# Performance work log

Hardware: AMD Instinct MI355X
Metric: run time of the kernel (lower is better)

The kernel has to match this reference:

```python
import jax, jax.numpy as jnp
import numpy as np

B = 1024          # graphs
NPG = 258         # nodes per graph (hard-coded in the model's reshape)
N = B * NPG
F_IN = 64
DEG = 8
E = B * NPG * DEG
CH = 32
HID = 128


def setup_inputs() -> dict:
    key = jax.random.key(0)
    ks = jax.random.split(key, 16)
    x = jax.random.normal(ks[0], (N, F_IN), dtype=jnp.float32)
    # within-graph random edges (disjoint batch): local idx in [0,258) + graph offset
    src_l = jax.random.randint(ks[1], (E,), 0, NPG, dtype=jnp.int32)
    dst_l = jax.random.randint(ks[2], (E,), 0, NPG, dtype=jnp.int32)
    offs = jnp.repeat(jnp.arange(B, dtype=jnp.int32) * NPG, NPG * DEG)
    edge_src = src_l + offs
    edge_dst = dst_l + offs
    edge_w = jax.random.uniform(ks[3], (E,), dtype=jnp.float32)
    s = lambda f: 1.0 / np.sqrt(f)
    W0 = jax.random.normal(ks[4], (F_IN, CH), dtype=jnp.float32) * s(F_IN)
    W1 = jax.random.normal(ks[5], (F_IN, CH), dtype=jnp.float32) * s(F_IN)
    b_conv = jnp.zeros((CH,), dtype=jnp.float32)
    Wd1 = jax.random.normal(ks[6], (NPG * CH, HID), dtype=jnp.float32) * s(NPG * CH)
    bd1 = jnp.zeros((HID,), dtype=jnp.float32)
    Wd2 = jax.random.normal(ks[7], (HID, HID // 2), dtype=jnp.float32) * s(HID)
    bd2 = jnp.zeros((HID // 2,), dtype=jnp.float32)
    Wd3 = jax.random.normal(ks[8], (HID // 2, HID // 4), dtype=jnp.float32) * s(HID // 2)
    bd3 = jnp.zeros((HID // 4,), dtype=jnp.float32)
    Wd4 = jax.random.normal(ks[9], (HID // 4, 1), dtype=jnp.float32) * s(HID // 4)
    bd4 = jnp.zeros((1,), dtype=jnp.float32)
    return dict(x=x, edge_src=edge_src, edge_dst=edge_dst, edge_w=edge_w,
                W0=W0, W1=W1, b_conv=b_conv, Wd1=Wd1, bd1=bd1, Wd2=Wd2, bd2=bd2,
                Wd3=Wd3, bd3=bd3, Wd4=Wd4, bd4=bd4)


def reference(x, edge_src, edge_dst, edge_w, W0, W1, b_conv,
              Wd1, bd1, Wd2, bd2, Wd3, bd3, Wd4, bd4):
    n = x.shape[0]
    # ChebConv K=2: T0 = X, T1 = A_hat X ; out = T0 W0 + T1 W1 + b, elu
    ax = jax.ops.segment_sum(edge_w[:, None] * x[edge_src], edge_dst, num_segments=n)
    h = jax.nn.elu(x @ W0 + ax @ W1 + b_conv)          # [N, 32]
    h = h.reshape(n // NPG, NPG * CH)                   # [B, 258*32] (reshape+flatten)
    h = jax.nn.relu(h @ Wd1 + bd1)
    h = jax.nn.relu(h @ Wd2 + bd2)
    # dropout is inactive at inference
    h = jax.nn.relu(h @ Wd3 + bd3)
    out = jax.nn.sigmoid(h @ Wd4 + bd4)                 # [B, 1]
    return out
```

## Files before the change

kernel.cpp:

```cpp
#include <hip/hip_runtime.h>
#include <hip/hip_bf16.h>

#define NPG 258
#define DEG 8
#define EPG 2064
#define CH 32
#define FIN 64
#define NB 1024
#define NTOT (NB * NPG)
#define HID 128
#define KTOT 8256
#define KSPL 32

typedef __attribute__((ext_vector_type(8))) short bf16x8;
typedef __attribute__((ext_vector_type(4))) float f32x4;

__device__ inline unsigned short f2bf(float f) {
    __hip_bfloat16 b = __float2bfloat16(f);
    return __builtin_bit_cast(unsigned short, b);
}
__device__ inline float bf2f(unsigned short u) {
    return __builtin_bit_cast(float, (unsigned)u << 16);
}
__device__ inline void cvt_split(const float4 a, const float4 b, bf16x8& hi, bf16x8& lo) {
    float f[8] = {a.x, a.y, a.z, a.w, b.x, b.y, b.z, b.w};
#pragma unroll
    for (int j = 0; j < 8; ++j) {
        unsigned short h = f2bf(f[j]);
        hi[j] = (short)h;
        lo[j] = (short)f2bf(f[j] - bf2f(h));
    }
}

__global__ __launch_bounds__(256) void prep_wcat(
    const float* __restrict__ W0, const float* __restrict__ W1,
    unsigned short* __restrict__ Wh, unsigned short* __restrict__ Wl)
{
#pragma unroll
    for (int i = 0; i < 16; ++i) {
        const int idx = threadIdx.x + i * 256;
        const int c = idx >> 6, k = idx & 63;
        const float v = (c < 32) ? W0[k * CH + c] : W1[k * CH + (c - 32)];
        const unsigned short h = f2bf(v);
        Wh[c * 64 + k] = h;
        Wl[c * 64 + k] = f2bf(v - bf2f(h));
    }
}

__global__ __launch_bounds__(256) void wd1_transpose(
    const float* __restrict__ Wd1, unsigned short* __restrict__ Wd1T)
{
    __shared__ float st[128][65];
    const int tid = threadIdx.x;
    const int k0 = blockIdx.x * 64;
#pragma unroll
    for (int i = 0; i < 32; ++i) {
        const int idx = tid + i * 256;
        const int kl = idx >> 7, cc = idx & 127;
        st[cc][kl] = Wd1[(size_t)(k0 + kl) * HID + cc];
    }
    __syncthreads();
    const int cc = tid >> 1, gq = tid & 1;
#pragma unroll
    for (int i = 0; i < 8; ++i) {
        const int ko = (gq + i * 2) * 4;
        ushort4 o;
        o.x = f2bf(st[cc][ko + 0]);
        o.y = f2bf(st[cc][ko + 1]);
        o.z = f2bf(st[cc][ko + 2]);
        o.w = f2bf(st[cc][ko + 3]);
        *reinterpret_cast<ushort4*>(Wd1T + (size_t)cc * KTOT + k0 + ko) = o;
    }
}

__global__ __launch_bounds__(256) void conv_gemm(
    const float* __restrict__ x, const unsigned short* __restrict__ Wh,
    const unsigned short* __restrict__ Wl,
    float* __restrict__ y0, unsigned short* __restrict__ y1)
{
    __shared__ unsigned short bsh[64 * 64];
    __shared__ unsigned short bsl[64 * 64];
    const int tid = threadIdx.x;
#pragma unroll
    for (int i = 0; i < 2; ++i) {
        const int s = tid + i * 256;
        const int col = s >> 3, o = s & 7;
        const int so = o ^ (col & 7);
        *reinterpret_cast<uint4*>(&bsh[col * 64 + so * 8]) =
            *reinterpret_cast<const uint4*>(&Wh[col * 64 + o * 8]);
        *reinterpret_cast<uint4*>(&bsl[col * 64 + so * 8]) =
            *reinterpret_cast<const uint4*>(&Wl[col * 64 + o * 8]);
    }
    __syncthreads();

    const int w = tid >> 6, lane = tid & 63;
    const int r = lane & 15, kq = lane >> 4;
    const long rowbase = (long)blockIdx.x * 128 + w * 32;

    bf16x8 ah[2][2], al[2][2];
#pragma unroll
    for (int mt = 0; mt < 2; ++mt)
#pragma unroll
        for (int ks = 0; ks < 2; ++ks) {
            const float* xp = x + (rowbase + mt * 16 + r) * FIN + ks * 32 + kq * 8;
            const float4 p0 = *reinterpret_cast<const float4*>(xp);
            const float4 p1 = *reinterpret_cast<const float4*>(xp + 4);
            cvt_split(p0, p1, ah[mt][ks], al[mt][ks]);
        }

    f32x4 acc[2][4];
#pragma unroll
    for (int mt = 0; mt < 2; ++mt)
#pragma unroll
        for (int nt = 0; nt < 4; ++nt) acc[mt][nt] = f32x4{0.f, 0.f, 0.f, 0.f};

#pragma unroll
    for (int nt = 0; nt < 4; ++nt) {
        const int col = nt * 16 + r;
        const int cs = col & 7;
#pragma unroll
        for (int ks = 0; ks < 2; ++ks) {
            const int g = (ks * 4 + kq) ^ cs;
            const bf16x8 bh = *reinterpret_cast<const bf16x8*>(&bsh[col * 64 + g * 8]);
            const bf16x8 bl = *reinterpret_cast<const bf16x8*>(&bsl[col * 64 + g * 8]);
#pragma unroll
            for (int mt = 0; mt < 2; ++mt) {
                acc[mt][nt] = __builtin_amdgcn_mfma_f32_16x16x32_bf16(ah[mt][ks], bh, acc[mt][nt], 0, 0, 0);
                acc[mt][nt] = __builtin_amdgcn_mfma_f32_16x16x32_bf16(ah[mt][ks], bl, acc[mt][nt], 0, 0, 0);
                acc[mt][nt] = __builtin_amdgcn_mfma_f32_16x16x32_bf16(al[mt][ks], bh, acc[mt][nt], 0, 0, 0);
            }
        }
    }

#pragma unroll
    for (int mt = 0; mt < 2; ++mt)
#pragma unroll
        for (int rr = 0; rr < 4; ++rr) {
            const long rg = rowbase + mt * 16 + kq * 4 + rr;
            y0[rg * CH + r]      = acc[mt][0][rr];
            y0[rg * CH + 16 + r] = acc[mt][1][rr];
            y1[rg * CH + r]      = f2bf(acc[mt][2][rr]);
            y1[rg * CH + 16 + r] = f2bf(acc[mt][3][rr]);
        }
}

__global__ __launch_bounds__(256) void conv_gather(
    const int* __restrict__ esrc, const int* __restrict__ edst,
    const float* __restrict__ ew, const float* __restrict__ y0,
    const unsigned short* __restrict__ y1, const float* __restrict__ bc,
    unsigned short* __restrict__ h)
{
    __shared__ unsigned short y1s[NPG * CH];
    __shared__ unsigned short slot_src[EPG];
    __shared__ float          slot_w[EPG];
    __shared__ int            row_start[NPG + 2];
    __shared__ int            cursor[NPG];

    const int g   = blockIdx.x;
    const int tid = threadIdx.x;
    const int n0  = g * NPG;
    const long eb = (long)g * EPG;
    const long qb = (long)g * (NPG * CH);

    if (tid < NPG) cursor[tid] = 0;
    if (tid + 256 < NPG) cursor[tid + 256] = 0;
    __syncthreads();

    for (int e = tid; e < EPG; e += 256)
        atomicAdd(&cursor[edst[eb + e] - n0], 1);
#pragma unroll
    for (int i = 0; i < 5; ++i) {
        const int q = tid + i * 256;
        if (q < 1032)
            *reinterpret_cast<uint4*>(&y1s[q * 8]) =
                *reinterpret_cast<const uint4*>(&y1[qb + (long)q * 8]);
    }
    __syncthreads();

    if (tid < 64) {
        const int b0 = tid * 5;
        int loc[5], s = 0;
#pragma unroll
        for (int j = 0; j < 5; ++j) {
            const int idx = b0 + j;
            loc[j] = (idx < NPG) ? cursor[idx] : 0;
            s += loc[j];
        }
        int inc = s;
#pragma unroll
        for (int off = 1; off < 64; off <<= 1) {
            const int t = __shfl_up(inc, off, 64);
            if (tid >= off) inc += t;
        }
        int run = inc - s;
#pragma unroll
        for (int j = 0; j < 5; ++j) {
            const int idx = b0 + j;
            if (idx < NPG) { row_start[idx] = run; cursor[idx] = run; }
            run += loc[j];
        }
        if (tid == 63) row_start[NPG] = inc;
    }
    __syncthreads();

    for (int e = tid; e < EPG; e += 256) {
        const int dl = edst[eb + e] - n0;
        const int sl = esrc[eb + e] - n0;
        const float w = ew[eb + e];
        const int pos = atomicAdd(&cursor[dl], 1);
        slot_src[pos] = (unsigned short)sl;
        slot_w[pos] = w;
    }
    __syncthreads();

    const int c = tid & 31;
    const int rgrp = tid >> 5;
#pragma unroll 1
    for (int p = 0; p < 33; ++p) {
        const int n = p * 8 + rgrp;
        if (n >= NPG) break;
        const int pb = row_start[n], pe = row_start[n + 1];
        float acc = 0.f;
        for (int pos = pb; pos < pe; ++pos)
            acc += slot_w[pos] * bf2f(y1s[slot_src[pos] * CH + c]);
        float v = y0[qb + (long)n * CH + c] + bc[c] + acc;
        v = (v > 0.f) ? v : expm1f(v);
        h[qb + (long)n * CH + c] = f2bf(v);
    }
}

__global__ __launch_bounds__(256) void gemm1(
    const unsigned short* __restrict__ h, const unsigned short* __restrict__ Wd1T,
    float* __restrict__ part)
{
    const int tid = threadIdx.x, w = tid >> 6, lane = tid & 63;
    const int r = lane & 15, kq = lane >> 4;
    const long m0 = (long)blockIdx.x * 64;
    const int ks = blockIdx.y;
    const int kb0 = ks * 258 / KSPL, kb1 = (ks + 1) * 258 / KSPL;
    const int c0 = w * 32;

    f32x4 acc[4][2];
#pragma unroll
    for (int a = 0; a < 4; ++a)
#pragma unroll
        for (int b = 0; b < 2; ++b) acc[a][b] = f32x4{0.f, 0.f, 0.f, 0.f};

    const unsigned short* ap = h    + (m0 + r) * KTOT + kq * 8;
    const unsigned short* bp = Wd1T + (long)(c0 + r) * KTOT + kq * 8;

    for (int kb = kb0; kb < kb1; ++kb) {
        const int k = kb * 32;
        const bf16x8 b0 = *reinterpret_cast<const bf16x8*>(bp + k);
        const bf16x8 b1 = *reinterpret_cast<const bf16x8*>(bp + 16 * KTOT + k);
#pragma unroll
        for (int mt = 0; mt < 4; ++mt) {
            const bf16x8 a = *reinterpret_cast<const bf16x8*>(ap + mt * 16 * KTOT + k);
            acc[mt][0] = __builtin_amdgcn_mfma_f32_16x16x32_bf16(a, b0, acc[mt][0], 0, 0, 0);
            acc[mt][1] = __builtin_amdgcn_mfma_f32_16x16x32_bf16(a, b1, acc[mt][1], 0, 0, 0);
        }
    }

    float* p = part + ((long)ks * NB + m0) * HID + c0;
#pragma unroll
    for (int mt = 0; mt < 4; ++mt)
#pragma unroll
        for (int rr = 0; rr < 4; ++rr) {
            const int row = mt * 16 + kq * 4 + rr;
            p[(long)row * HID + r]      = acc[mt][0][rr];
            p[(long)row * HID + 16 + r] = acc[mt][1][rr];
        }
}

__global__ __launch_bounds__(256) void mlp_tail(
    const float* __restrict__ part, const float* __restrict__ bd1,
    const float* __restrict__ Wd2, const float* __restrict__ bd2,
    const float* __restrict__ Wd3, const float* __restrict__ bd3,
    const float* __restrict__ Wd4, const float* __restrict__ bd4,
    float* __restrict__ out)
{
    __shared__ float w2[128 * 64];
    __shared__ float w3[64 * 32];
    __shared__ float w4[32];
    __shared__ float h1s[4][128];
    __shared__ float h2s[4][64];
    __shared__ float h3s[4][32];

    const int tid = threadIdx.x;
    for (int i = tid; i < 128 * 64; i += 256) w2[i] = Wd2[i];
    for (int i = tid; i < 64 * 32; i += 256)  w3[i] = Wd3[i];
    if (tid < 32) w4[tid] = Wd4[tid];

    const int r = tid >> 6;
    const int lane = tid & 63;
    const int row = blockIdx.x * 4 + r;

    float s0 = bd1[lane], s1 = bd1[lane + 64];
#pragma unroll 8
    for (int s = 0; s < KSPL; ++s) {
        const float* p = part + ((long)s * NB + row) * HID;
        s0 += p[lane];
        s1 += p[lane + 64];
    }
    h1s[r][lane]      = fmaxf(s0, 0.f);
    h1s[r][lane + 64] = fmaxf(s1, 0.f);
    __syncthreads();

    float s2 = bd2[lane];
#pragma unroll 8
    for (int k = 0; k < 128; ++k) s2 += h1s[r][k] * w2[k * 64 + lane];
    h2s[r][lane] = fmaxf(s2, 0.f);
    __syncthreads();

    if (lane < 32) {
        float s3 = bd3[lane];
#pragma unroll 8
        for (int k = 0; k < 64; ++k) s3 += h2s[r][k] * w3[k * 32 + lane];
        h3s[r][lane] = fmaxf(s3, 0.f);
    }
    __syncthreads();

    float p4 = (lane < 32) ? h3s[r][lane] * w4[lane] : 0.f;
#pragma unroll
    for (int off = 32; off > 0; off >>= 1) p4 += __shfl_down(p4, off, 64);
    if (lane == 0) out[row] = 1.f / (1.f + expf(-(p4 + bd4[0])));
}

extern "C" void kernel_launch(void* const* d_in, const int* in_sizes, int n_in,
                              void* d_out, int out_size, void* d_ws, size_t ws_size,
                              hipStream_t stream)
{
    const float* x    = (const float*)d_in[0];
    const int*   esrc = (const int*)d_in[1];
    const int*   edst = (const int*)d_in[2];
    const float* ew   = (const float*)d_in[3];
    const float* W0   = (const float*)d_in[4];
    const float* W1   = (const float*)d_in[5];
    const float* bc   = (const float*)d_in[6];
    const float* Wd1  = (const float*)d_in[7];
    const float* bd1  = (const float*)d_in[8];
    const float* Wd2  = (const float*)d_in[9];
    const float* bd2  = (const float*)d_in[10];
    const float* Wd3  = (const float*)d_in[11];
    const float* bd3  = (const float*)d_in[12];
    const float* Wd4  = (const float*)d_in[13];
    const float* bd4  = (const float*)d_in[14];
    float* out = (float*)d_out;

    char* wsb = (char*)d_ws;
    unsigned short* h    = (unsigned short*)wsb;
    unsigned short* wd1t = (unsigned short*)(wsb + 16908288);
    unsigned short* wch  = (unsigned short*)(wsb + 19021824);
    unsigned short* wcl  = (unsigned short*)(wsb + 19030016);
    float*          y0   = (float*)(wsb + 19038208);
    unsigned short* y1   = (unsigned short*)(wsb + 52854784);
    float*          part = (float*)(wsb + 19038208);

    prep_wcat<<<1, 256, 0, stream>>>(W0, W1, wch, wcl);
    wd1_transpose<<<KTOT / 64, 256, 0, stream>>>(Wd1, wd1t);
    conv_gemm<<<NTOT / 128, 256, 0, stream>>>(x, wch, wcl, y0, y1);
    conv_gather<<<NB, 256, 0, stream>>>(esrc, edst, ew, y0, y1, bc, h);
    gemm1<<<dim3(NB / 64, KSPL), 256, 0, stream>>>(h, wd1t, part);
    mlp_tail<<<NB / 4, 256, 0, stream>>>(part, bd1, Wd2, bd2, Wd3, bd3, Wd4, bd4, out);
}
```

Measured before the change: 230.5 us.

## Fuse conv GEMM with edge gather per graph, keeping y0/y1 in LDS

Merges the per-node feature GEMM and the per-graph edge aggregation into one 512-thread kernel per graph, so the y0/y1 intermediates stay in shared memory and never go through global memory. Edge data is loaded once into registers and reused for both the counting and scatter passes. The two weight-prep kernels are also merged into one launch, and the gather now processes two channels per thread. The cost is a larger LDS footprint per block (roughly 65KB), which lowers occupancy, and some MFMA work is wasted on padded rows because each graph has 258 nodes.

```diff
diff --git a/kernel.cpp b/kernel.cpp
--- a/kernel.cpp
+++ b/kernel.cpp
@@ -32,27 +32,26 @@
     }
 }
 
-__global__ __launch_bounds__(256) void prep_wcat(
+__global__ __launch_bounds__(256) void prep(
     const float* __restrict__ W0, const float* __restrict__ W1,
-    unsigned short* __restrict__ Wh, unsigned short* __restrict__ Wl)
-{
-#pragma unroll
-    for (int i = 0; i < 16; ++i) {
-        const int idx = threadIdx.x + i * 256;
-        const int c = idx >> 6, k = idx & 63;
-        const float v = (c < 32) ? W0[k * CH + c] : W1[k * CH + (c - 32)];
-        const unsigned short h = f2bf(v);
-        Wh[c * 64 + k] = h;
-        Wl[c * 64 + k] = f2bf(v - bf2f(h));
-    }
-}
-
-__global__ __launch_bounds__(256) void wd1_transpose(
+    unsigned short* __restrict__ Wh, unsigned short* __restrict__ Wl,
     const float* __restrict__ Wd1, unsigned short* __restrict__ Wd1T)
 {
+    const int tid = threadIdx.x;
+    if (blockIdx.x == 0) {
+#pragma unroll
+        for (int i = 0; i < 16; ++i) {
+            const int idx = tid + i * 256;
+            const int c = idx >> 6, k = idx & 63;
+            const float v = (c < 32) ? W0[k * CH + c] : W1[k * CH + (c - 32)];
+            const unsigned short h = f2bf(v);
+            Wh[c * 64 + k] = h;
+            Wl[c * 64 + k] = f2bf(v - bf2f(h));
+        }
+        return;
+    }
     __shared__ float st[128][65];
-    const int tid = threadIdx.x;
-    const int k0 = blockIdx.x * 64;
+    const int k0 = (blockIdx.x - 1) * 64;
 #pragma unroll
     for (int i = 0; i < 32; ++i) {
         const int idx = tid + i * 256;
@@ -73,107 +72,100 @@
     }
 }
 
-__global__ __launch_bounds__(256) void conv_gemm(
-    const float* __restrict__ x, const unsigned short* __restrict__ Wh,
-    const unsigned short* __restrict__ Wl,
-    float* __restrict__ y0, unsigned short* __restrict__ y1)
-{
+__global__ __launch_bounds__(512, 4) void conv_fused(
+    const float* __restrict__ x, const int* __restrict__ esrc,
+    const int* __restrict__ edst, const float* __restrict__ ew,
+    const unsigned short* __restrict__ Wh, const unsigned short* __restrict__ Wl,
+    const float* __restrict__ bc, unsigned short* __restrict__ h)
+{
+    __shared__ float          y0s[NPG * CH];
+    __shared__ unsigned short y1s[NPG * CH];
     __shared__ unsigned short bsh[64 * 64];
     __shared__ unsigned short bsl[64 * 64];
+    __shared__ unsigned short slot_src[EPG];
+    __shared__ float          slot_w[EPG];
+    __shared__ int            row_start[NPG + 1];
+    __shared__ int            cursor[NPG];
+
+    const int g   = blockIdx.x;
     const int tid = threadIdx.x;
-#pragma unroll
-    for (int i = 0; i < 2; ++i) {
-        const int s = tid + i * 256;
-        const int col = s >> 3, o = s & 7;
+    const int n0  = g * NPG;
+    const long eb = (long)g * EPG;
+    const long qb = (long)g * (NPG * CH);
+
+    {
+        const int col = tid >> 3, o = tid & 7;
         const int so = o ^ (col & 7);
         *reinterpret_cast<uint4*>(&bsh[col * 64 + so * 8]) =
             *reinterpret_cast<const uint4*>(&Wh[col * 64 + o * 8]);
         *reinterpret_cast<uint4*>(&bsl[col * 64 + so * 8]) =
             *reinterpret_cast<const uint4*>(&Wl[col * 64 + o * 8]);
     }
-    __syncthreads();
+    if (tid < NPG) cursor[tid] = 0;
+    __syncthreads();
+
+    unsigned e_u[4];
+    float    e_wv[4];
+#pragma unroll
+    for (int i = 0; i < 4; ++i) {
+        const int e = tid + i * 512;
+        const int sl = esrc[eb + e] - n0;
+        const int dl = edst[eb + e] - n0;
+        e_u[i] = (unsigned)sl | ((unsigned)dl << 16);
+        e_wv[i] = ew[eb + e];
+        atomicAdd(&cursor[dl], 1);
+    }
+    unsigned e_u4 = 0; float e_w4 = 0.f;
+    const bool has4 = (tid < EPG - 2048);
+    if (has4) {
+        const int e = tid + 2048;
+        const int sl = esrc[eb + e] - n0;
+        const int dl = edst[eb + e] - n0;
+        e_u4 = (unsigned)sl | ((unsigned)dl << 16);
+        e_w4 = ew[eb + e];
+        atomicAdd(&cursor[dl], 1);
+    }
 
     const int w = tid >> 6, lane = tid & 63;
     const int r = lane & 15, kq = lane >> 4;
-    const long rowbase = (long)blockIdx.x * 128 + w * 32;
-
-    bf16x8 ah[2][2], al[2][2];
-#pragma unroll
-    for (int mt = 0; mt < 2; ++mt)
+    for (int t = w; t < 17; t += 8) {
+        const int rbase = t * 16;
+        const int rowc = min(rbase + r, NPG - 1);
+        const float* xp = x + (long)(n0 + rowc) * FIN + kq * 8;
+        bf16x8 ah[2], al[2];
 #pragma unroll
         for (int ks = 0; ks < 2; ++ks) {
-            const float* xp = x + (rowbase + mt * 16 + r) * FIN + ks * 32 + kq * 8;
-            const float4 p0 = *reinterpret_cast<const float4*>(xp);
-            const float4 p1 = *reinterpret_cast<const float4*>(xp + 4);
-            cvt_split(p0, p1, ah[mt][ks], al[mt][ks]);
-        }
-
-    f32x4 acc[2][4];
-#pragma unroll
-    for (int mt = 0; mt < 2; ++mt)
-#pragma unroll
-        for (int nt = 0; nt < 4; ++nt) acc[mt][nt] = f32x4{0.f, 0.f, 0.f, 0.f};
-
-#pragma unroll
-    for (int nt = 0; nt < 4; ++nt) {
-        const int col = nt * 16 + r;
-        const int cs = col & 7;
-#pragma unroll
-        for (int ks = 0; ks < 2; ++ks) {
-            const int g = (ks * 4 + kq) ^ cs;
-            const bf16x8 bh = *reinterpret_cast<const bf16x8*>(&bsh[col * 64 + g * 8]);
-            const bf16x8 bl = *reinterpret_cast<const bf16x8*>(&bsl[col * 64 + g * 8]);
-#pragma unroll
-            for (int mt = 0; mt < 2; ++mt) {
-                acc[mt][nt] = __builtin_amdgcn_mfma_f32_16x16x32_bf16(ah[mt][ks], bh, acc[mt][nt], 0, 0, 0);
-                acc[mt][nt] = __builtin_amdgcn_mfma_f32_16x16x32_bf16(ah[mt][ks], bl, acc[mt][nt], 0, 0, 0);
-                acc[mt][nt] = __builtin_amdgcn_mfma_f32_16x16x32_bf16(al[mt][ks], bh, acc[mt][nt], 0, 0, 0);
+            const float4 p0 = *reinterpret_cast<const float4*>(xp + ks * 32);
+            const float4 p1 = *reinterpret_cast<const float4*>(xp + ks * 32 + 4);
+            cvt_split(p0, p1, ah[ks], al[ks]);
+        }
+        f32x4 acc[4];
+#pragma unroll
+        for (int nt = 0; nt < 4; ++nt) acc[nt] = f32x4{0.f, 0.f, 0.f, 0.f};
+#pragma unroll
+        for (int nt = 0; nt < 4; ++nt) {
+            const int col = nt * 16 + r;
+            const int cs = col & 7;
+#pragma unroll
+            for (int ks = 0; ks < 2; ++ks) {
+                const int gg = (ks * 4 + kq) ^ cs;
+                const bf16x8 bh = *reinterpret_cast<const bf16x8*>(&bsh[col * 64 + gg * 8]);
+                const bf16x8 bl = *reinterpret_cast<const bf16x8*>(&bsl[col * 64 + gg * 8]);
+                acc[nt] = __builtin_amdgcn_mfma_f32_16x16x32_bf16(ah[ks], bh, acc[nt], 0, 0, 0);
+                acc[nt] = __builtin_amdgcn_mfma_f32_16x16x32_bf16(ah[ks], bl, acc[nt], 0, 0, 0);
+                acc[nt] = __builtin_amdgcn_mfma_f32_16x16x32_bf16(al[ks], bh, acc[nt], 0, 0, 0);
             }
         }
-    }
-
-#pragma unroll
-    for (int mt = 0; mt < 2; ++mt)
 #pragma unroll
         for (int rr = 0; rr < 4; ++rr) {
-            const long rg = rowbase + mt * 16 + kq * 4 + rr;
-            y0[rg * CH + r]      = acc[mt][0][rr];
-            y0[rg * CH + 16 + r] = acc[mt][1][rr];
-            y1[rg * CH + r]      = f2bf(acc[mt][2][rr]);
-            y1[rg * CH + 16 + r] = f2bf(acc[mt][3][rr]);
-        }
-}
-
-__global__ __launch_bounds__(256) void conv_gather(
-    const int* __restrict__ esrc, const int* __restrict__ edst,
-    const float* __restrict__ ew, const float* __restrict__ y0,
-    const unsigned short* __restrict__ y1, const float* __restrict__ bc,
-    unsigned short* __restrict__ h)
-{
-    __shared__ unsigned short y1s[NPG * CH];
-    __shared__ unsigned short slot_src[EPG];
-    __shared__ float          slot_w[EPG];
-    __shared__ int            row_start[NPG + 2];
-    __shared__ int            cursor[NPG];
-
-    const int g   = blockIdx.x;
-    const int tid = threadIdx.x;
-    const int n0  = g * NPG;
-    const long eb = (long)g * EPG;
-    const long qb = (long)g * (NPG * CH);
-
-    if (tid < NPG) cursor[tid] = 0;
-    if (tid + 256 < NPG) cursor[tid + 256] = 0;
-    __syncthreads();
-
-    for (int e = tid; e < EPG; e += 256)
-        atomicAdd(&cursor[edst[eb + e] - n0], 1);
-#pragma unroll
-    for (int i = 0; i < 5; ++i) {
-        const int q = tid + i * 256;
-        if (q < 1032)
-            *reinterpret_cast<uint4*>(&y1s[q * 8]) =
-                *reinterpret_cast<const uint4*>(&y1[qb + (long)q * 8]);
+            const int row = rbase + kq * 4 + rr;
+            if (row < NPG) {
+                y0s[row * CH + r]      = acc[0][rr];
+                y0s[row * CH + 16 + r] = acc[1][rr];
+                y1s[row * CH + r]      = f2bf(acc[2][rr]);
+                y1s[row * CH + 16 + r] = f2bf(acc[3][rr]);
+            }
+        }
     }
     __syncthreads();
 
@@ -189,8 +181,8 @@
         int inc = s;
 #pragma unroll
         for (int off = 1; off < 64; off <<= 1) {
-            const int t = __shfl_up(inc, off, 64);
-            if (tid >= off) inc += t;
+            const int tshf = __shfl_up(inc, off, 64);
+            if (tid >= off) inc += tshf;
         }
         int run = inc - s;
 #pragma unroll
@@ -203,29 +195,43 @@
     }
     __syncthreads();
 
-    for (int e = tid; e < EPG; e += 256) {
-        const int dl = edst[eb + e] - n0;
-        const int sl = esrc[eb + e] - n0;
-        const float w = ew[eb + e];
+#pragma unroll
+    for (int i = 0; i < 4; ++i) {
+        const int dl = e_u[i] >> 16;
         const int pos = atomicAdd(&cursor[dl], 1);
-        slot_src[pos] = (unsigned short)sl;
-        slot_w[pos] = w;
-    }
-    __syncthreads();
-
-    const int c = tid & 31;
-    const int rgrp = tid >> 5;
+        slot_src[pos] = (unsigned short)(e_u[i] & 0xFFFFu);
+        slot_w[pos] = e_wv[i];
+    }
+    if (has4) {
+        const int dl = e_u4 >> 16;
+        const int pos = atomicAdd(&cursor[dl], 1);
+        slot_src[pos] = (unsigned short)(e_u4 & 0xFFFFu);
+        slot_w[pos] = e_w4;
+    }
+    __syncthreads();
+
+    const int grp = tid >> 4;
+    const int c = (tid & 15) * 2;
+    const float b0 = bc[c], b1 = bc[c + 1];
 #pragma unroll 1
-    for (int p = 0; p < 33; ++p) {
-        const int n = p * 8 + rgrp;
+    for (int p = 0; p < 9; ++p) {
+        const int n = p * 32 + grp;
         if (n >= NPG) break;
         const int pb = row_start[n], pe = row_start[n + 1];
-        float acc = 0.f;
-        for (int pos = pb; pos < pe; ++pos)
-            acc += slot_w[pos] * bf2f(y1s[slot_src[pos] * CH + c]);
-        float v = y0[qb + (long)n * CH + c] + bc[c] + acc;
-        v = (v > 0.f) ? v : expm1f(v);
-        h[qb + (long)n * CH + c] = f2bf(v);
+        float a0 = 0.f, a1 = 0.f;
+        for (int pos = pb; pos < pe; ++pos) {
+            const float wv = slot_w[pos];
+            const unsigned u = *reinterpret_cast<const unsigned*>(
+                &y1s[slot_src[pos] * CH + c]);
+            a0 += wv * bf2f((unsigned short)(u & 0xFFFFu));
+            a1 += wv * bf2f((unsigned short)(u >> 16));
+        }
+        float v0 = y0s[n * CH + c] + b0 + a0;
+        float v1 = y0s[n * CH + c + 1] + b1 + a1;
+        v0 = (v0 > 0.f) ? v0 : expm1f(v0);
+        v1 = (v1 > 0.f) ? v1 : expm1f(v1);
+        const unsigned o = (unsigned)f2bf(v0) | ((unsigned)f2bf(v1) << 16);
+        *reinterpret_cast<unsigned*>(&h[qb + (long)n * CH + c]) = o;
     }
 }
 
@@ -352,14 +358,10 @@
     unsigned short* wd1t = (unsigned short*)(wsb + 16908288);
     unsigned short* wch  = (unsigned short*)(wsb + 19021824);
     unsigned short* wcl  = (unsigned short*)(wsb + 19030016);
-    float*          y0   = (float*)(wsb + 19038208);
-    unsigned short* y1   = (unsigned short*)(wsb + 52854784);
     float*          part = (float*)(wsb + 19038208);
 
-    prep_wcat<<<1, 256, 0, stream>>>(W0, W1, wch, wcl);
-    wd1_transpose<<<KTOT / 64, 256, 0, stream>>>(Wd1, wd1t);
-    conv_gemm<<<NTOT / 128, 256, 0, stream>>>(x, wch, wcl, y0, y1);
-    conv_gather<<<NB, 256, 0, stream>>>(esrc, edst, ew, y0, y1, bc, h);
+    prep<<<1 + KTOT / 64, 256, 0, stream>>>(W0, W1, wch, wcl, Wd1, wd1t);
+    conv_fused<<<NB, 512, 0, stream>>>(x, esrc, edst, ew, wch, wcl, bc, h);
     gemm1<<<dim3(NB / 64, KSPL), 256, 0, stream>>>(h, wd1t, part);
     mlp_tail<<<NB / 4, 256, 0, stream>>>(part, bd1, Wd2, bd2, Wd3, bd3, Wd4, bd4, out);
 }
```

Result: faster. 196.9 us (-14.6%).
